# Optimization experiments

Hardware: AMD Instinct MI355X
Metric: run time of the kernel (lower is better)

Reference implementation:

```python
import jax, jax.numpy as jnp
import numpy as np

N = 50000   # nodes
IN = 256    # in_dim == hidden_dim
HID = 256
H = 4       # heads
HD = 64     # head_dim = HID // H
L = 2       # layers
E = 20000   # hyperedges
M = 320000  # incidence pairs
TQ = 64     # type_query_dim


def setup_inputs() -> dict:
    key = jax.random.key(0)
    ks = jax.random.split(key, 12)
    s = 0.05
    return {
        "x": jax.random.normal(ks[0], (N, IN), jnp.float32),
        "node_types": jax.random.randint(ks[1], (N,), 0, 3),
        "edge_type": jax.random.randint(ks[2], (E,), 0, 3),
        "node_idx": jax.random.randint(ks[3], (M,), 0, N),
        "edge_idx": jax.random.randint(ks[4], (M,), 0, E),
        # stacked per-layer, per-head parameters
        "tq": jax.random.normal(ks[5], (L, H, 3, TQ), jnp.float32) * s,      # type_query embedding
        "w1": jax.random.normal(ks[6], (L, H, 32, IN + TQ), jnp.float32) * s,  # type_attention_fc[0]
        "b1": jnp.zeros((L, H, 32), jnp.float32),
        "w2": jax.random.normal(ks[7], (L, H, 32), jnp.float32) * s,          # type_attention_fc[2]
        "b2": jnp.zeros((L, H), jnp.float32),
        "wq": jax.random.normal(ks[8], (L, H, HD, IN), jnp.float32) * s,      # query (no bias)
        "wv": jax.random.normal(ks[9], (L, H, HD, IN), jnp.float32) * s,      # value (no bias)
        "ec": jax.random.normal(ks[10], (L, H, 3, HD), jnp.float32) * s,      # edge_context embedding
        "ln_g": jnp.ones((L, HID), jnp.float32),
        "ln_b": jnp.zeros((L, HID), jnp.float32),
    }


def reference(x, node_types, edge_type, node_idx, edge_idx,
              tq, w1, b1, w2, b2, wq, wv, ec, ln_g, ln_b):
    h = x
    et_pair = edge_type[edge_idx]  # [M] edge type per incidence pair
    for l in range(L):
        # --- per-node type gate (alpha_type) ---
        sigs = jnp.moveaxis(tq[l], 0, 1)[node_types]                     # [N,H,TQ]
        hid = jnp.tanh(jnp.einsum('nd,hkd->nhk', h, w1[l, :, :, :IN])
                       + jnp.einsum('nhd,hkd->nhk', sigs, w1[l, :, :, IN:])
                       + b1[l][None])                                    # [N,H,32]
        alpha_type = jax.nn.sigmoid(jnp.einsum('nhk,hk->nh', hid, w2[l]) + b2[l][None])  # [N,H]
        # --- Q/V projections ---
        Q = jnp.einsum('nd,hod->nho', h, wq[l])                          # [N,H,HD]
        V = jnp.einsum('nd,hod->nho', h, wv[l])                          # [N,H,HD]
        ctx = jnp.moveaxis(ec[l], 0, 1)[et_pair]                         # [M,H,HD]
        # --- per-incidence attention logits ---
        alpha = jax.nn.leaky_relu(jnp.einsum('mho,mho->mh', Q[node_idx], ctx), 0.2)
        alpha = alpha * alpha_type[node_idx]                             # [M,H]
        # --- segment softmax over edges ---
        mx = jax.ops.segment_max(alpha, edge_idx, num_segments=E)        # [E,H]
        ex = jnp.exp(alpha - mx[edge_idx])
        den = jax.ops.segment_sum(ex, edge_idx, num_segments=E)
        attn = ex / den[edge_idx]                                        # [M,H]
        # --- dual scatter-add: node->edge then edge->node ---
        edge_feat = jax.ops.segment_sum(attn[:, :, None] * V[node_idx], edge_idx, num_segments=E)   # [E,H,HD]
        node_feat = jax.ops.segment_sum(attn[:, :, None] * edge_feat[edge_idx], node_idx, num_segments=N)  # [N,H,HD]
        # skip (identity since in_dim==hidden) + residual + LayerNorm
        h = h + node_feat.reshape(N, HID)
        mu = jnp.mean(h, -1, keepdims=True)
        var = jnp.mean((h - mu) ** 2, -1, keepdims=True)
        h = (h - mu) * jax.lax.rsqrt(var + 1e-5) * ln_g[l] + ln_b[l]
    return h
```

## Files before the change

### kernel.cpp

```cpp
#include <hip/hip_runtime.h>
#include <hip/hip_bf16.h>

typedef __hip_bfloat16 bf16;
using short8  = __attribute__((ext_vector_type(8))) short;
using float4v = __attribute__((ext_vector_type(4))) float;

static constexpr int N_ = 50000;
static constexpr int E_ = 20000;
static constexpr int M_ = 320000;
static constexpr int NPAD_ = 50048;
static constexpr int NB_E = (E_+255)/256;
static constexpr int NB_N = (N_+255)/256;
static constexpr int CVTB_ = 6250;
static constexpr int HISTB_ = 1250;
static constexpr int CVTALLB_ = 1364;
static constexpr int NREP_ = 8;

__device__ __forceinline__ float b2f(bf16 v){ return __bfloat162float(v); }
__device__ __forceinline__ float sigm(float x){ return 1.f/(1.f+__expf(-x)); }
__device__ __forceinline__ float u2f(unsigned short u){ return __uint_as_float(((unsigned)u)<<16); }
__device__ __forceinline__ unsigned short f2u(float f){ bf16 t=__float2bfloat16(f); return *(unsigned short*)&t; }

__global__ __launch_bounds__(256) void k_sniffzero(const unsigned short* __restrict__ xb, int* flag,
                                                   int* cnt_e, int* cnt_n){
  int b = blockIdx.x, tid = threadIdx.x;
  if (b == 0){
    int sane = 0;
    for (int i = tid; i < 4096; i += 256){
      unsigned short u = xb[2*i];
      int ex = (u >> 7) & 0xFF;
      if ((u & 0x7FFF) == 0 || (ex >= 117 && ex <= 137)) sane++;
    }
    #pragma unroll
    for (int d=1; d<64; d<<=1) sane += __shfl_xor(sane, d, 64);
    __shared__ int wsh[4];
    if ((tid&63)==0) wsh[tid>>6] = sane;
    __syncthreads();
    if (tid==0){
      int tot = wsh[0]+wsh[1]+wsh[2]+wsh[3];
      *flag = (tot > 2048) ? 1 : 0;
    }
  } else {
    int i = (b-1)*256 + tid;
    if (i < NREP_*E_) cnt_e[i] = 0;
    else if (i < NREP_*E_ + NREP_*N_) cnt_n[i - NREP_*E_] = 0;
  }
}

__global__ __launch_bounds__(256) void k_prep(
    const void* __restrict__ x, bf16* __restrict__ h16,
    const void* s0, const void* s1, const void* s2, const void* s3, const void* s4,
    const void* s5, const void* s6, const void* s7, const void* s8, const void* s9,
    float* d0, float* d1, float* d2, float* d3, float* d4,
    float* d5, float* d6, float* d7, float* d8, float* d9,
    const int* __restrict__ eidx, const int* __restrict__ nidx,
    int* cnt_e, int* cnt_n,
    const int* __restrict__ flag){
  int b = blockIdx.x, t = threadIdx.x;
  if (b < HISTB_){
    int m = b*256 + t;
    int rep = b & (NREP_-1);
    if (m < M_){
      atomicAdd(&cnt_e[rep*E_ + eidx[m]],1);
      atomicAdd(&cnt_n[rep*N_ + nidx[m]],1);
    }
    return;
  }
  if (b < HISTB_+CVTALLB_){
    int i = (b-HISTB_)*256 + t;
    const void* src; float* dst; int off;
    if      (i < 1536)            { src=s0; dst=d0; off=i; }
    else if (i < 1536+81920)      { src=s1; dst=d1; off=i-1536; }
    else if (i < 83712+256)       { src=s2; dst=d2; off=i-83712; }
    else if (i < 83968+256)       { src=s3; dst=d3; off=i-83968; }
    else if (i < 84224+8)         { src=s4; dst=d4; off=i-84224; }
    else if (i < 84232+131072)    { src=s5; dst=d5; off=i-84232; }
    else if (i < 215304+131072)   { src=s6; dst=d6; off=i-215304; }
    else if (i < 346376+1536)     { src=s7; dst=d7; off=i-346376; }
    else if (i < 347912+512)      { src=s8; dst=d8; off=i-347912; }
    else if (i < 348424+512)      { src=s9; dst=d9; off=i-348424; }
    else return;
    if (*flag) dst[off] = b2f(((const bf16*)src)[off]);
    else       dst[off] = ((const float*)src)[off];
    return;
  }
  size_t i0 = ((size_t)(b-(HISTB_+CVTALLB_))*256 + t) * 8;
  if (*flag){
    short8 v = *(const short8*)((const unsigned short*)x + i0);
    *(short8*)(h16 + i0) = v;
  } else {
    const float* xf = (const float*)x + i0;
    float4 a = *(const float4*)xf;
    float4 c = *(const float4*)(xf + 4);
    short8 v;
    v[0]=(short)f2u(a.x); v[1]=(short)f2u(a.y); v[2]=(short)f2u(a.z); v[3]=(short)f2u(a.w);
    v[4]=(short)f2u(c.x); v[5]=(short)f2u(c.y); v[6]=(short)f2u(c.z); v[7]=(short)f2u(c.w);
    *(short8*)(h16 + i0) = v;
  }
}

__device__ __forceinline__ void scan1_body(const int* cnt, int* off, int* bsum, int n, int blk){
  int tid = threadIdx.x, lane = tid&63, wid = tid>>6;
  int i = blk*256 + tid;
  int v = 0;
  if (i < n){
    #pragma unroll
    for (int c=0;c<NREP_;++c) v += cnt[c*n + i];
  }
  int s = v;
  #pragma unroll
  for (int d=1; d<64; d<<=1){ int t = __shfl_up(s, d, 64); if (lane>=d) s += t; }
  __shared__ int ws[4]; __shared__ int wo[4];
  if (lane==63) ws[wid] = s;
  __syncthreads();
  if (tid==0){ int a=0; for (int k=0;k<4;k++){ int t=ws[k]; wo[k]=a; a+=t; } bsum[blk]=a; }
  __syncthreads();
  if (i<n) off[i] = wo[wid] + s - v;
}

__global__ __launch_bounds__(256) void k_scan1w(
    const int* __restrict__ cnt_e, int* __restrict__ eoff, int* bsum_e,
    const int* __restrict__ cnt_n, int* __restrict__ noff, int* bsum_n,
    const float* __restrict__ tq_f, const float* __restrict__ w1_f, const float* __restrict__ b1_f,
    float* __restrict__ pre,
    const float* __restrict__ wv_f, const float* __restrict__ wq_f, const float* __restrict__ ec_f,
    bf16* __restrict__ Bp){
  int b = blockIdx.x;
  if (b < NB_E){ scan1_body(cnt_e, eoff, bsum_e, E_, b); return; }
  if (b < NB_E+NB_N){ scan1_body(cnt_n, noff, bsum_n, N_, b-NB_E); return; }
  int b2 = b - (NB_E+NB_N);
  if (b2 < 3){
    int idx = b2*256 + threadIdx.x;
    if (idx >= 768) return;
    int l = idx / 384, r = idx % 384;
    int t = r / 128, r2 = r % 128;
    int h = r2 >> 5, k = r2 & 31;
    const float* tp = tq_f + ((l*4+h)*3 + t)*64;
    const float* wp = w1_f + (size_t)((l*4+h)*32 + k)*320 + 256;
    float s = b1_f[(l*4+h)*32 + k];
    for (int d=0; d<64; ++d) s += tp[d]*wp[d];
    pre[(l*3+t)*128 + r2] = s;
    return;
  }
  int idx = (b2-3)*256 + threadIdx.x;
  if (idx >= 2*448*256) return;
  int l = idx / (448*256), r = idx % (448*256);
  int c = r >> 8, k = r & 255;
  float v = 0.f;
  if (c < 256){
    int dd = c >> 2, h = c & 3;
    v = wv_f[(size_t)l*65536 + (size_t)(h*64+dd)*256 + k];
  }
  else if (c < 384) v = w1_f[(size_t)l*40960 + (size_t)(c-256)*320 + k];
  else if (c < 396){
    int ht = c-384, h = ht/3, tt = ht%3;
    const float* ecp = ec_f + ((l*4+h)*3 + tt)*64;
    const float* wqp = wq_f + (size_t)((l*4+h)*64)*256 + k;
    float s = 0.f;
    for (int o2=0; o2<64; ++o2) s += ecp[o2]*wqp[(size_t)o2*256];
    v = s;
  }
  Bp[idx] = __float2bfloat16(v);
}

__global__ __launch_bounds__(256) void k_scan23(const int* __restrict__ bsum_e, int* __restrict__ eoff, int* cur_e,
                                                const int* __restrict__ bsum_n, int* __restrict__ noff, int* cur_n){
  int b = blockIdx.x, t = threadIdx.x, lane = t&63, wid = t>>6;
  int nb, n, blk;
  const int* bsum; int* off; int* cur;
  if (b < NB_E){ nb=NB_E; n=E_; bsum=bsum_e; off=eoff; cur=cur_e; blk=b; }
  else         { nb=NB_N; n=N_; bsum=bsum_n; off=noff; cur=cur_n; blk=b-NB_E; }
  int v = (t < blk) ? bsum[t] : 0;
  #pragma unroll
  for (int d=1; d<64; d<<=1) v += __shfl_xor(v, d, 64);
  __shared__ int ws[4];
  if (lane==0) ws[wid] = v;
  __syncthreads();
  int p = ws[0]+ws[1]+ws[2]+ws[3];
  int i = blk*256 + t;
  if (i < n){ int e = off[i] + p; off[i] = e; cur[i] = e; }
  if (blk == nb-1 && t == 0) off[n] = p + bsum[nb-1];
}

__global__ __launch_bounds__(256) void k_fill(const int* __restrict__ eidx, const int* __restrict__ nidx,
                                              int* cur_e, int* cur_n, int* ep, int* np){
  int m = blockIdx.x*256 + threadIdx.x;
  if (m < M_){
    int p = atomicAdd(&cur_e[eidx[m]],1); ep[p]=m;
    int q = atomicAdd(&cur_n[nidx[m]],1); np[q]=m;
  }
}

__global__ __launch_bounds__(256,3) void k_mgemm(const bf16* __restrict__ A16, const bf16* __restrict__ Bp,
    bf16* __restrict__ V16, bf16* __restrict__ Hb16, float* __restrict__ S){
  int g = blockIdx.x;
  int xcd = g & 7, i7 = g >> 3;
  int wgid = (xcd==0) ? i7 : (343 + (xcd-1)*342 + i7);
  int x = wgid % 7, y = wgid / 7;

  int t = threadIdx.x;
  int wid = t >> 6, lane = t & 63;
  int q = lane >> 4, li = lane & 15;
  int row0blk = y*128;
  int col0 = x*64;
  int w32 = wid*32;

  __shared__ char lds[49152];

  float4v acc[2][4];
  #pragma unroll
  for (int i=0;i<2;i++)
    #pragma unroll
    for (int j=0;j<4;j++) acc[i][j] = (float4v)(0.f);

  auto stage = [&](int st, int buf){
    const int k0 = st*64;
    char* lA = lds + (buf ? 24576 : 0);
    char* lB = lds + (buf ? 40960 : 16384);
    const bf16* Asrc = A16 + (size_t)row0blk*256 + k0;
    const bf16* Bsrc = Bp  + (size_t)col0*256 + k0;
    #pragma unroll
    for (int ra=0; ra<4; ++ra){
      int gidx = ra*256 + t;
      int r = gidx >> 3, c = gidx & 7;
      const bf16* src = Asrc + (size_t)r*256 + ((c ^ (r&7)) << 3);
      char* dst = lA + (ra*256 + wid*64)*16;
      __builtin_amdgcn_global_load_lds((const __attribute__((address_space(1))) void*)src,
                                       (__attribute__((address_space(3))) void*)dst, 16, 0, 0);
    }
    #pragma unroll
    for (int rb=0; rb<2; ++rb){
      int gidx = rb*256 + t;
      int r = gidx >> 3, c = gidx & 7;
      const bf16* src = Bsrc + (size_t)r*256 + ((c ^ (r&7)) << 3);
      char* dst = lB + (rb*256 + wid*64)*16;
      __builtin_amdgcn_global_load_lds((const __attribute__((address_space(1))) void*)src,
                                       (__attribute__((address_space(3))) void*)dst, 16, 0, 0);
    }
  };

  stage(0, 0);
  #pragma unroll
  for (int st=0; st<4; ++st){
    int bufc = st & 1;
    if (st < 3) stage(st+1, bufc^1);
    __builtin_amdgcn_sched_barrier(0);
    if (st < 3) asm volatile("s_waitcnt vmcnt(6)" ::: "memory");
    else        asm volatile("s_waitcnt vmcnt(0)" ::: "memory");
    __builtin_amdgcn_s_barrier();
    __builtin_amdgcn_sched_barrier(0);

    const char* cA = lds + (bufc ? 24576 : 0);
    const char* cB = lds + (bufc ? 40960 : 16384);
    short8 af[2][2], bfr[4][2];
    #pragma unroll
    for (int i=0;i<2;i++)
      #pragma unroll
      for (int k2=0;k2<2;k2++){
        int row = w32 + i*16 + li;
        int gr = (k2*4 + q) ^ (li & 7);
        af[i][k2] = *(const short8*)(cA + row*128 + gr*16);
      }
    #pragma unroll
    for (int j=0;j<4;j++)
      #pragma unroll
      for (int k2=0;k2<2;k2++){
        int row = j*16 + li;
        int gr = (k2*4 + q) ^ (li & 7);
        bfr[j][k2] = *(const short8*)(cB + row*128 + gr*16);
      }
    #pragma unroll
    for (int k2=0;k2<2;k2++)
      #pragma unroll
      for (int j=0;j<4;j++){
        acc[0][j] = __builtin_amdgcn_mfma_f32_16x16x32_bf16(af[0][k2], bfr[j][k2], acc[0][j],0,0,0);
        acc[1][j] = __builtin_amdgcn_mfma_f32_16x16x32_bf16(af[1][k2], bfr[j][k2], acc[1][j],0,0,0);
      }
    __builtin_amdgcn_sched_barrier(0);
    __builtin_amdgcn_s_barrier();
  }

  int row0 = row0blk + w32;
  #pragma unroll
  for (int i=0;i<2;i++){
    #pragma unroll
    for (int r=0;r<4;r++){
      int grow = row0 + i*16 + q*4 + r;
      if (grow >= N_) continue;
      #pragma unroll
      for (int j=0;j<4;j++){
        int gc = col0 + j*16 + li;
        float v = acc[i][j][r];
        if (gc < 256)      V16 [(size_t)grow*256 + gc]       = __float2bfloat16(v);
        else if (gc < 384) Hb16[(size_t)grow*128 + gc - 256] = __float2bfloat16(v);
        else if (gc < 396) S   [(size_t)grow*12  + gc - 384] = v;
      }
    }
  }
}

__global__ __launch_bounds__(256) void k_gate(const unsigned short* __restrict__ Hb16, const float* __restrict__ S,
    const float* __restrict__ pre_l, const float* __restrict__ w2_l, const float* __restrict__ b2_l,
    const int* __restrict__ ntype, float* __restrict__ G){
  int node = blockIdx.x*4 + (threadIdx.x>>6);
  int lane = threadIdx.x & 63;
  if (node >= N_) return;
  int typ = ntype[node];
  const float* pr = pre_l + typ*128;
  float v0 = tanhf(u2f(Hb16[(size_t)node*128 + lane])      + pr[lane]);
  float v1 = tanhf(u2f(Hb16[(size_t)node*128 + 64 + lane]) + pr[64+lane]);
  float p0 = v0 * w2_l[lane];
  float p1 = v1 * w2_l[64+lane];
  #pragma unroll
  for (int d=1; d<32; d<<=1){ p0 += __shfl_xor(p0,d,64); p1 += __shfl_xor(p1,d,64); }
  float at0 = sigm(__shfl(p0, 0,64) + b2_l[0]);
  float at1 = sigm(__shfl(p0,32,64) + b2_l[1]);
  float at2 = sigm(__shfl(p1, 0,64) + b2_l[2]);
  float at3 = sigm(__shfl(p1,32,64) + b2_l[3]);
  if (lane < 12){
    int h = lane / 3, t = lane % 3;
    float sv = S[(size_t)node*12 + lane];
    float lr = (sv > 0.f) ? sv : 0.2f*sv;
    float av = (h==0)? at0 : (h==1)? at1 : (h==2)? at2 : at3;
    G[(size_t)node*12 + t*4 + h] = lr * av;
  }
}

__global__ __launch_bounds__(256) void k_edge(const int* __restrict__ eoff, const int* __restrict__ ep,
    const int* __restrict__ nidx, const int* __restrict__ etype,
    const float* __restrict__ G, const unsigned short* __restrict__ V16,
    float* __restrict__ attn, unsigned short* __restrict__ EF16){
  int e = blockIdx.x*4 + (threadIdx.x>>6);
  int lane = threadIdx.x & 63;
  if (e >= E_) return;
  int beg = eoff[e], end = eoff[e+1];
  int deg = end - beg;
  if (deg == 0) return;
  int t = etype[e];
  float a0=0,a1=0,a2=0,a3=0;

  if (deg <= 64){
    int i = beg + lane;
    int m = -1, n = 0;
    float4 g; g.x=g.y=g.z=g.w=-1e30f;
    if (lane < deg){
      m = ep[i]; n = nidx[m];
      g = *(const float4*)(G + (size_t)n*12 + t*4);
    }
    float mx0=g.x, mx1=g.y, mx2=g.z, mx3=g.w;
    #pragma unroll
    for (int d=1; d<64; d<<=1){
      mx0=fmaxf(mx0,__shfl_xor(mx0,d,64)); mx1=fmaxf(mx1,__shfl_xor(mx1,d,64));
      mx2=fmaxf(mx2,__shfl_xor(mx2,d,64)); mx3=fmaxf(mx3,__shfl_xor(mx3,d,64));
    }
    float ex0=0,ex1=0,ex2=0,ex3=0;
    if (lane < deg){
      ex0=__expf(g.x-mx0); ex1=__expf(g.y-mx1); ex2=__expf(g.z-mx2); ex3=__expf(g.w-mx3);
    }
    float s0=ex0,s1=ex1,s2=ex2,s3=ex3;
    #pragma unroll
    for (int d=1; d<64; d<<=1){
      s0+=__shfl_xor(s0,d,64); s1+=__shfl_xor(s1,d,64);
      s2+=__shfl_xor(s2,d,64); s3+=__shfl_xor(s3,d,64);
    }
    float4 w; w.x=ex0/s0; w.y=ex1/s1; w.z=ex2/s2; w.w=ex3/s3;
    if (lane < deg) *(float4*)(attn + (size_t)m*4) = w;
    auto ldrow = [&](int j)->ushort4{
      int nn = __shfl(n, j, 64);
      return *(const ushort4*)(V16 + (size_t)nn*256 + (lane<<2));
    };
    ushort4 v0v,v1v,v2v,v3v,v4v,v5v,v6v,v7v;
    if (deg>0) v0v=ldrow(0);
    if (deg>1) v1v=ldrow(1);
    if (deg>2) v2v=ldrow(2);
    if (deg>3) v3v=ldrow(3);
    if (deg>4) v4v=ldrow(4);
    if (deg>5) v5v=ldrow(5);
    if (deg>6) v6v=ldrow(6);
    if (deg>7) v7v=ldrow(7);
    for (int j=0;j<deg;j+=8){
      { float wx=__shfl(w.x,j,64),wy=__shfl(w.y,j,64),wz=__shfl(w.z,j,64),wq=__shfl(w.w,j,64);
        a0+=wx*u2f(v0v.x); a1+=wy*u2f(v0v.y); a2+=wz*u2f(v0v.z); a3+=wq*u2f(v0v.w);
        if (j+8<deg) v0v=ldrow(j+8); }
      if (j+1<deg){
        float wx=__shfl(w.x,j+1,64),wy=__shfl(w.y,j+1,64),wz=__shfl(w.z,j+1,64),wq=__shfl(w.w,j+1,64);
        a0+=wx*u2f(v1v.x); a1+=wy*u2f(v1v.y); a2+=wz*u2f(v1v.z); a3+=wq*u2f(v1v.w);
        if (j+9<deg) v1v=ldrow(j+9); }
      if (j+2<deg){
        float wx=__shfl(w.x,j+2,64),wy=__shfl(w.y,j+2,64),wz=__shfl(w.z,j+2,64),wq=__shfl(w.w,j+2,64);
        a0+=wx*u2f(v2v.x); a1+=wy*u2f(v2v.y); a2+=wz*u2f(v2v.z); a3+=wq*u2f(v2v.w);
        if (j+10<deg) v2v=ldrow(j+10); }
      if (j+3<deg){
        float wx=__shfl(w.x,j+3,64),wy=__shfl(w.y,j+3,64),wz=__shfl(w.z,j+3,64),wq=__shfl(w.w,j+3,64);
        a0+=wx*u2f(v3v.x); a1+=wy*u2f(v3v.y); a2+=wz*u2f(v3v.z); a3+=wq*u2f(v3v.w);
        if (j+11<deg) v3v=ldrow(j+11); }
      if (j+4<deg){
        float wx=__shfl(w.x,j+4,64),wy=__shfl(w.y,j+4,64),wz=__shfl(w.z,j+4,64),wq=__shfl(w.w,j+4,64);
        a0+=wx*u2f(v4v.x); a1+=wy*u2f(v4v.y); a2+=wz*u2f(v4v.z); a3+=wq*u2f(v4v.w);
        if (j+12<deg) v4v=ldrow(j+12); }
      if (j+5<deg){
        float wx=__shfl(w.x,j+5,64),wy=__shfl(w.y,j+5,64),wz=__shfl(w.z,j+5,64),wq=__shfl(w.w,j+5,64);
        a0+=wx*u2f(v5v.x); a1+=wy*u2f(v5v.y); a2+=wz*u2f(v5v.z); a3+=wq*u2f(v5v.w);
        if (j+13<deg) v5v=ldrow(j+13); }
      if (j+6<deg){
        float wx=__shfl(w.x,j+6,64),wy=__shfl(w.y,j+6,64),wz=__shfl(w.z,j+6,64),wq=__shfl(w.w,j+6,64);
        a0+=wx*u2f(v6v.x); a1+=wy*u2f(v6v.y); a2+=wz*u2f(v6v.z); a3+=wq*u2f(v6v.w);
        if (j+14<deg) v6v=ldrow(j+14); }
      if (j+7<deg){
        float wx=__shfl(w.x,j+7,64),wy=__shfl(w.y,j+7,64),wz=__shfl(w.z,j+7,64),wq=__shfl(w.w,j+7,64);
        a0+=wx*u2f(v7v.x); a1+=wy*u2f(v7v.y); a2+=wz*u2f(v7v.z); a3+=wq*u2f(v7v.w);
        if (j+15<deg) v7v=ldrow(j+15); }
    }
  } else {
    float mx0=-1e30f, mx1=-1e30f, mx2=-1e30f, mx3=-1e30f;
    for (int i=beg+lane; i<end; i+=64){
      int m = ep[i]; int n = nidx[m];
      float4 g = *(const float4*)(G + (size_t)n*12 + t*4);
      mx0=fmaxf(mx0,g.x); mx1=fmaxf(mx1,g.y); mx2=fmaxf(mx2,g.z); mx3=fmaxf(mx3,g.w);
    }
    #pragma unroll
    for (int d=1; d<64; d<<=1){
      mx0=fmaxf(mx0,__shfl_xor(mx0,d,64)); mx1=fmaxf(mx1,__shfl_xor(mx1,d,64));
      mx2=fmaxf(mx2,__shfl_xor(mx2,d,64)); mx3=fmaxf(mx3,__shfl_xor(mx3,d,64));
    }
    float sm0=0,sm1=0,sm2=0,sm3=0;
    for (int i=beg+lane; i<end; i+=64){
      int m = ep[i]; int n = nidx[m];
      float4 g = *(const float4*)(G + (size_t)n*12 + t*4);
      sm0+=__expf(g.x-mx0); sm1+=__expf(g.y-mx1); sm2+=__expf(g.z-mx2); sm3+=__expf(g.w-mx3);
    }
    #pragma unroll
    for (int d=1; d<64; d<<=1){
      sm0+=__shfl_xor(sm0,d,64); sm1+=__shfl_xor(sm1,d,64);
      sm2+=__shfl_xor(sm2,d,64); sm3+=__shfl_xor(sm3,d,64);
    }
    float inv0=1.f/sm0, inv1=1.f/sm1, inv2=1.f/sm2, inv3=1.f/sm3;
    for (int i=beg+lane; i<end; i+=64){
      int m = ep[i]; int n = nidx[m];
      float4 g = *(const float4*)(G + (size_t)n*12 + t*4);
      float4 w;
      w.x=__expf(g.x-mx0)*inv0; w.y=__expf(g.y-mx1)*inv1;
      w.z=__expf(g.z-mx2)*inv2; w.w=__expf(g.w-mx3)*inv3;
      *(float4*)(attn + (size_t)m*4) = w;
    }
    for (int i=beg; i<end; ++i){
      int m = ep[i]; int n = nidx[m];
      float4 g = *(const float4*)(G + (size_t)n*12 + t*4);
      float w0=__expf(g.x-mx0)*inv0, w1=__expf(g.y-mx1)*inv1;
      float w2=__expf(g.z-mx2)*inv2, w3=__expf(g.w-mx3)*inv3;
      ushort4 v = *(const ushort4*)(V16 + (size_t)n*256 + lane*4);
      a0 += w0*u2f(v.x); a1 += w1*u2f(v.y); a2 += w2*u2f(v.z); a3 += w3*u2f(v.w);
    }
  }
  ushort4 ev; ev.x=f2u(a0); ev.y=f2u(a1); ev.z=f2u(a2); ev.w=f2u(a3);
  *(ushort4*)(EF16 + (size_t)e*256 + lane*4) = ev;
}

__global__ __launch_bounds__(256) void k_node(const int* __restrict__ noff, const int* __restrict__ np,
    const int* __restrict__ eidx, const float* __restrict__ attn, const unsigned short* __restrict__ EF16,
    const float* __restrict__ lng, const float* __restrict__ lnb,
    bf16* __restrict__ h16, void* __restrict__ outv, const int* __restrict__ flag, int last){
  int n = blockIdx.x*4 + (threadIdx.x>>6);
  int lane = threadIdx.x & 63;
  if (n >= N_) return;
  float f0=0,f1=0,f2=0,f3=0;
  int beg = noff[n], end = noff[n+1];
  int deg = end - beg;
  if (deg > 0 && deg <= 64){
    int i = beg + lane;
    int e = 0;
    float4 w; w.x=w.y=w.z=w.w=0.f;
    if (lane < deg){
      int m = np[i]; e = eidx[m];
      w = *(const float4*)(attn + (size_t)m*4);
    }
    auto ldrow = [&](int j)->ushort4{
      int ee = __shfl(e, j, 64);
      return *(const ushort4*)(EF16 + (size_t)ee*256 + (lane<<2));
    };
    ushort4 v0v,v1v,v2v,v3v,v4v,v5v,v6v,v7v;
    if (deg>0) v0v=ldrow(0);
    if (deg>1) v1v=ldrow(1);
    if (deg>2) v2v=ldrow(2);
    if (deg>3) v3v=ldrow(3);
    if (deg>4) v4v=ldrow(4);
    if (deg>5) v5v=ldrow(5);
    if (deg>6) v6v=ldrow(6);
    if (deg>7) v7v=ldrow(7);
    for (int j=0;j<deg;j+=8){
      { float wx=__shfl(w.x,j,64),wy=__shfl(w.y,j,64),wz=__shfl(w.z,j,64),wq=__shfl(w.w,j,64);
        f0+=wx*u2f(v0v.x); f1+=wy*u2f(v0v.y); f2+=wz*u2f(v0v.z); f3+=wq*u2f(v0v.w);
        if (j+8<deg) v0v=ldrow(j+8); }
      if (j+1<deg){
        float wx=__shfl(w.x,j+1,64),wy=__shfl(w.y,j+1,64),wz=__shfl(w.z,j+1,64),wq=__shfl(w.w,j+1,64);
        f0+=wx*u2f(v1v.x); f1+=wy*u2f(v1v.y); f2+=wz*u2f(v1v.z); f3+=wq*u2f(v1v.w);
        if (j+9<deg) v1v=ldrow(j+9); }
      if (j+2<deg){
        float wx=__shfl(w.x,j+2,64),wy=__shfl(w.y,j+2,64),wz=__shfl(w.z,j+2,64),wq=__shfl(w.w,j+2,64);
        f0+=wx*u2f(v2v.x); f1+=wy*u2f(v2v.y); f2+=wz*u2f(v2v.z); f3+=wq*u2f(v2v.w);
        if (j+10<deg) v2v=ldrow(j+10); }
      if (j+3<deg){
        float wx=__shfl(w.x,j+3,64),wy=__shfl(w.y,j+3,64),wz=__shfl(w.z,j+3,64),wq=__shfl(w.w,j+3,64);
        f0+=wx*u2f(v3v.x); f1+=wy*u2f(v3v.y); f2+=wz*u2f(v3v.z); f3+=wq*u2f(v3v.w);
        if (j+11<deg) v3v=ldrow(j+11); }
      if (j+4<deg){
        float wx=__shfl(w.x,j+4,64),wy=__shfl(w.y,j+4,64),wz=__shfl(w.z,j+4,64),wq=__shfl(w.w,j+4,64);
        f0+=wx*u2f(v4v.x); f1+=wy*u2f(v4v.y); f2+=wz*u2f(v4v.z); f3+=wq*u2f(v4v.w);
        if (j+12<deg) v4v=ldrow(j+12); }
      if (j+5<deg){
        float wx=__shfl(w.x,j+5,64),wy=__shfl(w.y,j+5,64),wz=__shfl(w.z,j+5,64),wq=__shfl(w.w,j+5,64);
        f0+=wx*u2f(v5v.x); f1+=wy*u2f(v5v.y); f2+=wz*u2f(v5v.z); f3+=wq*u2f(v5v.w);
        if (j+13<deg) v5v=ldrow(j+13); }
      if (j+6<deg){
        float wx=__shfl(w.x,j+6,64),wy=__shfl(w.y,j+6,64),wz=__shfl(w.z,j+6,64),wq=__shfl(w.w,j+6,64);
        f0+=wx*u2f(v6v.x); f1+=wy*u2f(v6v.y); f2+=wz*u2f(v6v.z); f3+=wq*u2f(v6v.w);
        if (j+14<deg) v6v=ldrow(j+14); }
      if (j+7<deg){
        float wx=__shfl(w.x,j+7,64),wy=__shfl(w.y,j+7,64),wz=__shfl(w.z,j+7,64),wq=__shfl(w.w,j+7,64);
        f0+=wx*u2f(v7v.x); f1+=wy*u2f(v7v.y); f2+=wz*u2f(v7v.z); f3+=wq*u2f(v7v.w);
        if (j+15<deg) v7v=ldrow(j+15); }
    }
  } else if (deg > 64){
    for (int i=beg; i<end; ++i){
      int m = np[i]; int e = eidx[m];
      float4 w = *(const float4*)(attn + (size_t)m*4);
      ushort4 v = *(const ushort4*)(EF16 + (size_t)e*256 + lane*4);
      f0 += w.x*u2f(v.x); f1 += w.y*u2f(v.y); f2 += w.z*u2f(v.z); f3 += w.w*u2f(v.w);
    }
  }
  const bf16* hp = h16 + (size_t)n*256;
  float h0 = b2f(hp[lane])+f0, h1 = b2f(hp[64+lane])+f1, h2 = b2f(hp[128+lane])+f2, h3 = b2f(hp[192+lane])+f3;
  float s = h0+h1+h2+h3;
  #pragma unroll
  for (int d=1; d<64; d<<=1) s += __shfl_xor(s,d,64);
  float mean = s * (1.f/256.f);
  float d0=h0-mean, d1=h1-mean, d2=h2-mean, d3=h3-mean;
  float vv = d0*d0+d1*d1+d2*d2+d3*d3;
  #pragma unroll
  for (int d=1; d<64; d<<=1) vv += __shfl_xor(vv,d,64);
  float rstd = rsqrtf(vv*(1.f/256.f) + 1e-5f);
  float o0 = d0*rstd*lng[lane]     + lnb[lane];
  float o1 = d1*rstd*lng[64+lane]  + lnb[64+lane];
  float o2 = d2*rstd*lng[128+lane] + lnb[128+lane];
  float o3 = d3*rstd*lng[192+lane] + lnb[192+lane];
  if (last){
    if (*flag){
      bf16* op = (bf16*)outv + (size_t)n*256;
      op[lane]=__float2bfloat16(o0); op[64+lane]=__float2bfloat16(o1);
      op[128+lane]=__float2bfloat16(o2); op[192+lane]=__float2bfloat16(o3);
    } else {
      float* op = (float*)outv + (size_t)n*256;
      op[lane]=o0; op[64+lane]=o1; op[128+lane]=o2; op[192+lane]=o3;
    }
  } else {
    bf16* o16 = h16 + (size_t)n*256;
    o16[lane]=__float2bfloat16(o0); o16[64+lane]=__float2bfloat16(o1);
    o16[128+lane]=__float2bfloat16(o2); o16[192+lane]=__float2bfloat16(o3);
  }
}

extern "C" void kernel_launch(void* const* d_in, const int* in_sizes, int n_in,
                              void* d_out, int out_size, void* d_ws, size_t ws_size,
                              hipStream_t stream){
  const void* x    = d_in[0];
  const int* ntype = (const int*)d_in[1];
  const int* etype = (const int*)d_in[2];
  const int* nidx  = (const int*)d_in[3];
  const int* eidx  = (const int*)d_in[4];
  (void)in_sizes; (void)n_in; (void)out_size; (void)ws_size;

  char* ws = (char*)d_ws;
  size_t o = 0;
  auto alloc = [&](size_t b)->char*{ char* r = ws + o; o = (o + b + 255) & ~(size_t)255; return r; };
  int*   flag = (int*)  alloc(256);
  char*  R2   =         alloc((size_t)20000000);
  float* G    = (float*)alloc((size_t)N_*12*4);
  float* tq_f  = (float*)alloc(1536*4);
  float* w1_f  = (float*)alloc(81920*4);
  float* b1_f  = (float*)alloc(256*4);
  float* w2_f  = (float*)alloc(256*4);
  float* b2_f  = (float*)alloc(8*4);
  float* wq_f  = (float*)alloc(131072*4);
  float* wv_f  = (float*)alloc(131072*4);
  float* ec_f  = (float*)alloc(1536*4);
  float* lng_f = (float*)alloc(512*4);
  float* lnb_f = (float*)alloc(512*4);
  float* pre   = (float*)alloc(768*4);
  int* cnt_e  = (int*)alloc((size_t)NREP_*E_*4);
  int* cnt_n  = (int*)alloc((size_t)NREP_*N_*4);
  int* eoff   = (int*)alloc((size_t)(E_+1)*4);
  int* noff   = (int*)alloc((size_t)(N_+1)*4);
  int* cur_e  = (int*)alloc((size_t)E_*4);
  int* cur_n  = (int*)alloc((size_t)N_*4);
  int* ep     = (int*)alloc((size_t)M_*4);
  int* np     = (int*)alloc((size_t)M_*4);
  int* bsum_e = (int*)alloc(256*4);
  int* bsum_n = (int*)alloc(256*4);
  bf16* h16   = (bf16*)alloc((size_t)NPAD_*256*2);
  bf16* Bp    = (bf16*)alloc((size_t)2*448*256*2);
  bf16* V16   = (bf16*)alloc((size_t)N_*256*2);

  bf16*  Hb16 = (bf16*)R2;
  float* S    = (float*)(R2 + 16777216);
  float* attn = (float*)R2;
  unsigned short* EF16 = (unsigned short*)(R2 + 5242880);

  k_sniffzero<<<1 + (NREP_*(E_+N_)+255)/256, 256, 0, stream>>>((const unsigned short*)x, flag, cnt_e, cnt_n);
  k_prep<<<HISTB_+CVTALLB_+CVTB_, 256, 0, stream>>>(
      x, h16,
      d_in[5], d_in[6], d_in[7], d_in[8], d_in[9],
      d_in[10], d_in[11], d_in[12], d_in[13], d_in[14],
      tq_f, w1_f, b1_f, w2_f, b2_f, wq_f, wv_f, ec_f, lng_f, lnb_f,
      eidx, nidx, cnt_e, cnt_n, flag);
  k_scan1w<<<NB_E+NB_N+3+896, 256, 0, stream>>>(
      cnt_e, eoff, bsum_e, cnt_n, noff, bsum_n,
      tq_f, w1_f, b1_f, pre, wv_f, wq_f, ec_f, Bp);
  k_scan23<<<NB_E+NB_N, 256, 0, stream>>>(bsum_e, eoff, cur_e, bsum_n, noff, cur_n);
  k_fill<<<M_/256, 256, 0, stream>>>(eidx, nidx, cur_e, cur_n, ep, np);

  for (int l=0; l<2; ++l){
    k_mgemm<<<2737, 256, 0, stream>>>(h16, Bp + (size_t)l*448*256, V16, Hb16, S);
    k_gate<<<12500, 256, 0, stream>>>((const unsigned short*)Hb16, S, pre + l*384,
                                      w2_f + l*128, b2_f + l*4, ntype, G);
    k_edge<<<5000, 256, 0, stream>>>(eoff, ep, nidx, etype, G, (const unsigned short*)V16, attn, EF16);
    k_node<<<12500, 256, 0, stream>>>(noff, np, eidx, attn, EF16, lng_f + l*256, lnb_f + l*256,
                                      h16, d_out, flag, l==1);
  }
}
```

Measured before the change: 437.7 us.

## Store incidence indices and attention in CSR-position order to remove double indirection

The fill kernel now records, for each edge-sorted slot, the node id and that incidence's position in the node-sorted order, plus the edge id for each node-sorted slot. The edge kernel writes attention weights directly in node-CSR order, so the node kernel reads attention and edge ids contiguously instead of chasing m through np and eidx. This removes dependent gather loads in both per-layer kernels. The cost is an extra M-sized index array, one more write in the fill step, and scattered attention writes in the edge kernel.

After: 427.6 us, median of 2. -2.3%, faster.

```diff
diff --git a/kernel.cpp b/kernel.cpp
--- a/kernel.cpp
+++ b/kernel.cpp
@@ -183,11 +183,16 @@
 }
 
 __global__ __launch_bounds__(256) void k_fill(const int* __restrict__ eidx, const int* __restrict__ nidx,
-                                              int* cur_e, int* cur_n, int* ep, int* np){
+                                              int* cur_e, int* cur_n,
+                                              int* nofp, int* qofp, int* en){
   int m = blockIdx.x*256 + threadIdx.x;
   if (m < M_){
-    int p = atomicAdd(&cur_e[eidx[m]],1); ep[p]=m;
-    int q = atomicAdd(&cur_n[nidx[m]],1); np[q]=m;
+    int e = eidx[m], n = nidx[m];
+    int p = atomicAdd(&cur_e[e],1);
+    int q = atomicAdd(&cur_n[n],1);
+    nofp[p] = n;
+    qofp[p] = q;
+    en[q]   = e;
   }
 }
 
@@ -326,10 +331,10 @@
   }
 }
 
-__global__ __launch_bounds__(256) void k_edge(const int* __restrict__ eoff, const int* __restrict__ ep,
-    const int* __restrict__ nidx, const int* __restrict__ etype,
+__global__ __launch_bounds__(256) void k_edge(const int* __restrict__ eoff,
+    const int* __restrict__ nofp, const int* __restrict__ qofp, const int* __restrict__ etype,
     const float* __restrict__ G, const unsigned short* __restrict__ V16,
-    float* __restrict__ attn, unsigned short* __restrict__ EF16){
+    float* __restrict__ attn_n, unsigned short* __restrict__ EF16){
   int e = blockIdx.x*4 + (threadIdx.x>>6);
   int lane = threadIdx.x & 63;
   if (e >= E_) return;
@@ -340,11 +345,10 @@
   float a0=0,a1=0,a2=0,a3=0;
 
   if (deg <= 64){
-    int i = beg + lane;
-    int m = -1, n = 0;
+    int n = 0;
     float4 g; g.x=g.y=g.z=g.w=-1e30f;
     if (lane < deg){
-      m = ep[i]; n = nidx[m];
+      n = nofp[beg + lane];
       g = *(const float4*)(G + (size_t)n*12 + t*4);
     }
     float mx0=g.x, mx1=g.y, mx2=g.z, mx3=g.w;
@@ -364,7 +368,10 @@
       s2+=__shfl_xor(s2,d,64); s3+=__shfl_xor(s3,d,64);
     }
     float4 w; w.x=ex0/s0; w.y=ex1/s1; w.z=ex2/s2; w.w=ex3/s3;
-    if (lane < deg) *(float4*)(attn + (size_t)m*4) = w;
+    if (lane < deg){
+      int q = qofp[beg + lane];
+      *(float4*)(attn_n + (size_t)q*4) = w;
+    }
     auto ldrow = [&](int j)->ushort4{
       int nn = __shfl(n, j, 64);
       return *(const ushort4*)(V16 + (size_t)nn*256 + (lane<<2));
@@ -414,7 +421,7 @@
   } else {
     float mx0=-1e30f, mx1=-1e30f, mx2=-1e30f, mx3=-1e30f;
     for (int i=beg+lane; i<end; i+=64){
-      int m = ep[i]; int n = nidx[m];
+      int n = nofp[i];
       float4 g = *(const float4*)(G + (size_t)n*12 + t*4);
       mx0=fmaxf(mx0,g.x); mx1=fmaxf(mx1,g.y); mx2=fmaxf(mx2,g.z); mx3=fmaxf(mx3,g.w);
     }
@@ -425,7 +432,7 @@
     }
     float sm0=0,sm1=0,sm2=0,sm3=0;
     for (int i=beg+lane; i<end; i+=64){
-      int m = ep[i]; int n = nidx[m];
+      int n = nofp[i];
       float4 g = *(const float4*)(G + (size_t)n*12 + t*4);
       sm0+=__expf(g.x-mx0); sm1+=__expf(g.y-mx1); sm2+=__expf(g.z-mx2); sm3+=__expf(g.w-mx3);
     }
@@ -436,15 +443,15 @@
     }
     float inv0=1.f/sm0, inv1=1.f/sm1, inv2=1.f/sm2, inv3=1.f/sm3;
     for (int i=beg+lane; i<end; i+=64){
-      int m = ep[i]; int n = nidx[m];
+      int n = nofp[i];
       float4 g = *(const float4*)(G + (size_t)n*12 + t*4);
       float4 w;
       w.x=__expf(g.x-mx0)*inv0; w.y=__expf(g.y-mx1)*inv1;
       w.z=__expf(g.z-mx2)*inv2; w.w=__expf(g.w-mx3)*inv3;
-      *(float4*)(attn + (size_t)m*4) = w;
+      *(float4*)(attn_n + (size_t)qofp[i]*4) = w;
     }
     for (int i=beg; i<end; ++i){
-      int m = ep[i]; int n = nidx[m];
+      int n = nofp[i];
       float4 g = *(const float4*)(G + (size_t)n*12 + t*4);
       float w0=__expf(g.x-mx0)*inv0, w1=__expf(g.y-mx1)*inv1;
       float w2=__expf(g.z-mx2)*inv2, w3=__expf(g.w-mx3)*inv3;
@@ -456,8 +463,8 @@
   *(ushort4*)(EF16 + (size_t)e*256 + lane*4) = ev;
 }
 
-__global__ __launch_bounds__(256) void k_node(const int* __restrict__ noff, const int* __restrict__ np,
-    const int* __restrict__ eidx, const float* __restrict__ attn, const unsigned short* __restrict__ EF16,
+__global__ __launch_bounds__(256) void k_node(const int* __restrict__ noff, const int* __restrict__ en,
+    const float* __restrict__ attn_n, const unsigned short* __restrict__ EF16,
     const float* __restrict__ lng, const float* __restrict__ lnb,
     bf16* __restrict__ h16, void* __restrict__ outv, const int* __restrict__ flag, int last){
   int n = blockIdx.x*4 + (threadIdx.x>>6);
@@ -471,8 +478,8 @@
     int e = 0;
     float4 w; w.x=w.y=w.z=w.w=0.f;
     if (lane < deg){
-      int m = np[i]; e = eidx[m];
-      w = *(const float4*)(attn + (size_t)m*4);
+      e = en[i];
+      w = *(const float4*)(attn_n + (size_t)i*4);
     }
     auto ldrow = [&](int j)->ushort4{
       int ee = __shfl(e, j, 64);
@@ -522,8 +529,8 @@
     }
   } else if (deg > 64){
     for (int i=beg; i<end; ++i){
-      int m = np[i]; int e = eidx[m];
-      float4 w = *(const float4*)(attn + (size_t)m*4);
+      int e = en[i];
+      float4 w = *(const float4*)(attn_n + (size_t)i*4);
       ushort4 v = *(const ushort4*)(EF16 + (size_t)e*256 + lane*4);
       f0 += w.x*u2f(v.x); f1 += w.y*u2f(v.y); f2 += w.z*u2f(v.z); f3 += w.w*u2f(v.w);
     }
@@ -592,8 +599,9 @@
   int* noff   = (int*)alloc((size_t)(N_+1)*4);
   int* cur_e  = (int*)alloc((size_t)E_*4);
   int* cur_n  = (int*)alloc((size_t)N_*4);
-  int* ep     = (int*)alloc((size_t)M_*4);
-  int* np     = (int*)alloc((size_t)M_*4);
+  int* nofp   = (int*)alloc((size_t)M_*4);
+  int* qofp   = (int*)alloc((size_t)M_*4);
+  int* en     = (int*)alloc((size_t)M_*4);
   int* bsum_e = (int*)alloc(256*4);
   int* bsum_n = (int*)alloc(256*4);
   bf16* h16   = (bf16*)alloc((size_t)NPAD_*256*2);
@@ -602,7 +610,7 @@
 
   bf16*  Hb16 = (bf16*)R2;
   float* S    = (float*)(R2 + 16777216);
-  float* attn = (float*)R2;
+  float* attn_n = (float*)R2;
   unsigned short* EF16 = (unsigned short*)(R2 + 5242880);
 
   k_sniffzero<<<1 + (NREP_*(E_+N_)+255)/256, 256, 0, stream>>>((const unsigned short*)x, flag, cnt_e, cnt_n);
@@ -616,14 +624,14 @@
       cnt_e, eoff, bsum_e, cnt_n, noff, bsum_n,
       tq_f, w1_f, b1_f, pre, wv_f, wq_f, ec_f, Bp);
   k_scan23<<<NB_E+NB_N, 256, 0, stream>>>(bsum_e, eoff, cur_e, bsum_n, noff, cur_n);
-  k_fill<<<M_/256, 256, 0, stream>>>(eidx, nidx, cur_e, cur_n, ep, np);
+  k_fill<<<M_/256, 256, 0, stream>>>(eidx, nidx, cur_e, cur_n, nofp, qofp, en);
 
   for (int l=0; l<2; ++l){
     k_mgemm<<<2737, 256, 0, stream>>>(h16, Bp + (size_t)l*448*256, V16, Hb16, S);
     k_gate<<<12500, 256, 0, stream>>>((const unsigned short*)Hb16, S, pre + l*384,
                                       w2_f + l*128, b2_f + l*4, ntype, G);
-    k_edge<<<5000, 256, 0, stream>>>(eoff, ep, nidx, etype, G, (const unsigned short*)V16, attn, EF16);
-    k_node<<<12500, 256, 0, stream>>>(noff, np, eidx, attn, EF16, lng_f + l*256, lnb_f + l*256,
+    k_edge<<<5000, 256, 0, stream>>>(eoff, nofp, qofp, etype, G, (const unsigned short*)V16, attn_n, EF16);
+    k_node<<<12500, 256, 0, stream>>>(noff, en, attn_n, EF16, lng_f + l*256, lnb_f + l*256,
                                       h16, d_out, flag, l==1);
   }
 }
```
